# Optimization experiments

Measured on AMD Instinct MI355X. Metric: run time of the kernel, lower is better.

Reference implementation:

```python
import jax, jax.numpy as jnp
import numpy as np

SOCIAL_IDS = (1, 18)
BN_EPS = 1e-5


def conv1d(x, w, b):
    # x: [N, C, L], w: [O, I, 3], padding=1
    y = jax.lax.conv_general_dilated(x, w, window_strides=(1,), padding=[(1, 1)],
                                     dimension_numbers=("NCH", "OIH", "NCH"))
    return y + b[None, :, None]


def batchnorm(x, gamma, beta):
    # training-mode BatchNorm1d: biased stats over (N, L)
    m = x.mean(axis=(0, 2), keepdims=True)
    v = ((x - m) ** 2).mean(axis=(0, 2), keepdims=True)
    return gamma[None, :, None] * (x - m) * jax.lax.rsqrt(v + BN_EPS) + beta[None, :, None]


def social_stats(activity_ids):
    # Vectorized run-length-encoding of the social mask (replaces the per-element Python loop).
    mask = (activity_ids == SOCIAL_IDS[0]) | (activity_ids == SOCIAL_IDS[1])  # [B, S]
    prev = jnp.pad(mask[:, :-1], ((0, 0), (1, 0)))
    starts = mask & ~prev
    nseg = starts.sum(-1).astype(jnp.float32)                 # sigma_frequency
    total_dur = mask.sum(-1).astype(jnp.float32)
    mu_dur = jnp.where(nseg > 0, total_dur / jnp.maximum(nseg, 1.0), 0.0)
    # gap positions: non-social with social both before and after -> exactly the inter-segment gaps
    cum = jnp.cumsum(mask, axis=-1)
    rcum = jnp.cumsum(mask[:, ::-1], axis=-1)[:, ::-1]
    gap_sum = ((~mask) & (cum > 0) & (rcum > 0)).sum(-1).astype(jnp.float32)
    resp = jnp.where(nseg > 1, gap_sum / jnp.maximum(nseg - 1.0, 1.0), 0.0)
    return jnp.stack([mu_dur, nseg, resp], axis=-1)          # [B, 3]


def compute_sws(cur, base):
    num = cur[:, 0] * cur[:, 1]
    den = base[:, 0] * base[:, 1] + 1e-10
    return jnp.clip(1.0 - num / den, 0.0, 1.0)


def setup_inputs() -> dict:
    key = jax.random.key(0)
    ks = jax.random.split(key, 16)
    B, S, D, V = 32, 8192, 128, 21
    inp = {
        "activity_ids": jax.random.randint(ks[0], (B, S), 0, V),
        "baseline_stats": jax.random.uniform(ks[1], (B, 3), dtype=jnp.float32) * 10.0 + 0.5,
        "embed": jax.random.normal(ks[2], (V, D), dtype=jnp.float32),
        "W1": jax.random.normal(ks[3], (256, D, 3), dtype=jnp.float32) * 0.05,
        "b1": jnp.zeros((256,), jnp.float32),
        "g1": jnp.ones((256,), jnp.float32),
        "be1": jnp.zeros((256,), jnp.float32),
        "W2": jax.random.normal(ks[4], (128, 256, 3), dtype=jnp.float32) * 0.05,
        "b2": jnp.zeros((128,), jnp.float32),
        "g2": jnp.ones((128,), jnp.float32),
        "be2": jnp.zeros((128,), jnp.float32),
        "W3": jax.random.normal(ks[5], (D, 128, 3), dtype=jnp.float32) * 0.05,
        "b3": jnp.zeros((D,), jnp.float32),
        "Ws": jax.random.normal(ks[6], (D, 3), dtype=jnp.float32) * 0.1,
        "bs": jnp.zeros((D,), jnp.float32),
        "Wo": jax.random.normal(ks[7], (D, 2 * D), dtype=jnp.float32) * 0.05,
        "bo": jnp.zeros((D,), jnp.float32),
    }
    return inp


def reference(activity_ids, baseline_stats, embed, W1, b1, g1, be1, W2, b2, g2, be2,
              W3, b3, Ws, bs, Wo, bo):
    x = embed[activity_ids]                   # [B, S, D]
    x = x.transpose(0, 2, 1)                  # [B, D, S]
    x = jax.nn.relu(batchnorm(conv1d(x, W1, b1), g1, be1))
    x = jax.nn.relu(batchnorm(conv1d(x, W2, b2), g2, be2))
    x = jax.nn.relu(conv1d(x, W3, b3))
    h_cnn = x.mean(axis=2)                    # [B, D]
    stats = social_stats(activity_ids)        # [B, 3]
    h_stats = stats @ Ws.T + bs               # [B, D]
    sws = compute_sws(stats, baseline_stats)  # [B]
    h = jnp.concatenate([h_cnn, h_stats], axis=-1)
    h_si = h @ Wo.T + bo                      # [B, D]
    return (h_si, sws)
```

## Files before the change

kernel.cpp:

```cpp
#include <hip/hip_runtime.h>
#include <hip/hip_bf16.h>
#include <cstdint>
#include <cstddef>

#define B_    32
#define S_    8192
#define D_    128
#define V_    21
#define VP_   22
#define T_    (VP_*VP_*VP_)
#define TPAD_ 10656
#define C1_   256
#define C2_   128
#define NPOS_ (B_*S_)
#define CH_   128
#define NCHUNK_ 64

using bf16x8 = __attribute__((ext_vector_type(8))) short;
using f32x4  = __attribute__((ext_vector_type(4))) float;
using u32x4  = __attribute__((ext_vector_type(4))) unsigned;

__device__ inline unsigned short f2bf(float f) {
  union { float f; unsigned u; } v; v.f = f;
  unsigned r = v.u + 0x7fffu + ((v.u >> 16) & 1u);
  return (unsigned short)(r >> 16);
}
__device__ inline float bf2f(unsigned short h) {
  union { unsigned u; float f; } v; v.u = ((unsigned)h) << 16; return v.f;
}

__global__ void k_prep(const float* __restrict__ W1, const float* __restrict__ emb,
                       const float* __restrict__ W2, const float* __restrict__ W3,
                       float* __restrict__ G, unsigned short* __restrict__ Wr2,
                       unsigned short* __restrict__ W3r,
                       const int* __restrict__ ids, int* __restrict__ tIdx,
                       int* __restrict__ cnt, int* __restrict__ socC,
                       int* __restrict__ socS, int* __restrict__ socF,
                       int* __restrict__ socL) {
  int bid = blockIdx.x;
  if (bid < 66) {
    int v = bid % VP_, k = bid / VP_, o = threadIdx.x;
    __shared__ float e[D_];
    if (o < D_) e[o] = (v < V_) ? emb[v * D_ + o] : 0.f;
    __syncthreads();
    float acc = 0.f;
    if (v < V_) {
      for (int i = 0; i < D_; ++i) acc += W1[o * (D_ * 3) + i * 3 + k] * e[i];
    }
    G[(k * VP_ + v) * C1_ + o] = acc;
    return;
  }
  if (bid < 834) {
    int idx = (bid - 66) * 256 + threadIdx.x;
    if (idx < 384 * 256) {
      int r = idx >> 8, o = idx & 255;
      int k = r >> 7, p = r & 127;
      Wr2[idx] = f2bf(W2[(p * C1_ + o) * 3 + k]);
    } else {
      int j = idx - 384 * 256;
      if (j < 128 * 384) {
        int q = j / 384, kk = j % 384;
        int k = kk >> 7, p = kk & 127;
        W3r[q * 384 + kk] = f2bf(W3[(q * C2_ + p) * 3 + k]);
      }
    }
    return;
  }
  int idx = (bid - 834) * 256 + threadIdx.x;
  int b = idx >> 13, s = idx & (S_ - 1);
  const int* row = ids + b * S_;
  int a = (s > 0)      ? row[s - 1] : V_;
  int m = row[s];
  int c = (s < S_ - 1) ? row[s + 1] : V_;
  int t = (a * VP_ + m) * VP_ + c;
  tIdx[idx] = t;
  atomicAdd(&cnt[t], 1);

  bool sm = (m == 1) | (m == 18);
  bool pm = (a == 1) | (a == 18);
  unsigned long long bm = __ballot(sm);
  unsigned long long bs = __ballot(sm && !pm);
  __shared__ int l0, l1, l2, l3;
  if (threadIdx.x == 0) { l0 = 0; l1 = 0; l2 = 0; l3 = 0; }
  __syncthreads();
  int lane = threadIdx.x & 63;
  int fc = sm ? (S_ - 1 - s) : 0;
  int lv = sm ? s : 0;
#pragma unroll
  for (int off = 1; off < 64; off <<= 1) {
    fc = max(fc, __shfl_xor(fc, off));
    lv = max(lv, __shfl_xor(lv, off));
  }
  if (lane == 0) {
    atomicAdd(&l0, (int)__popcll(bm));
    atomicAdd(&l1, (int)__popcll(bs));
    atomicMax(&l2, fc);
    atomicMax(&l3, lv);
  }
  __syncthreads();
  if (threadIdx.x == 0) {
    atomicAdd(&socC[b], l0); atomicAdd(&socS[b], l1);
    atomicMax(&socF[b], l2); atomicMax(&socL[b], l3);
  }
}

__global__ void k_stats1(const float* __restrict__ G, const float* __restrict__ b1,
                         const int* __restrict__ cnt,
                         float* __restrict__ m1acc, float* __restrict__ v1acc) {
  int o = threadIdx.x;
  float bb = b1[o];
  float s = 0.f, sq = 0.f;
  int t0 = blockIdx.x * 16;
#pragma unroll 4
  for (int i = 0; i < 16; ++i) {
    int t = t0 + i;
    if (t >= T_) break;
    int a = t / (VP_ * VP_), m = (t / VP_) % VP_, c = t % VP_;
    float x = G[a * C1_ + o] + G[(VP_ + m) * C1_ + o] + G[(2 * VP_ + c) * C1_ + o] + bb;
    float w = (float)cnt[t];
    s += w * x; sq += w * x * x;
  }
  atomicAdd(&m1acc[o], s);
  atomicAdd(&v1acc[o], sq);
}

__global__ void k_z1(const float* __restrict__ G, const float* __restrict__ b1,
                     const float* __restrict__ m1a, const float* __restrict__ v1a,
                     const float* __restrict__ g1, const float* __restrict__ be1,
                     unsigned* __restrict__ Z1u) {
  int tid = threadIdx.x;
  int t = blockIdx.x * 2 + (tid >> 7);
  int o = (tid & 127) * 2;
  float m0 = m1a[o] * (1.f / NPOS_), m1v = m1a[o + 1] * (1.f / NPOS_);
  float a0 = g1[o]     * rsqrtf(v1a[o]     * (1.f / NPOS_) - m0 * m0   + 1e-5f);
  float a1 = g1[o + 1] * rsqrtf(v1a[o + 1] * (1.f / NPOS_) - m1v * m1v + 1e-5f);
  float c0 = be1[o] - m0 * a0, c1 = be1[o + 1] - m1v * a1;
  unsigned pk = 0;
  if (t < T_) {
    int a = t / (VP_ * VP_), m = (t / VP_) % VP_, c = t % VP_;
    float2 xa = *(const float2*)(G + (size_t)a * C1_ + o);
    float2 xm = *(const float2*)(G + (size_t)(VP_ + m) * C1_ + o);
    float2 xc = *(const float2*)(G + (size_t)(2 * VP_ + c) * C1_ + o);
    float x0 = xa.x + xm.x + xc.x + b1[o];
    float x1 = xa.y + xm.y + xc.y + b1[o + 1];
    float z0 = fmaxf(a0 * x0 + c0, 0.f);
    float z1 = fmaxf(a1 * x1 + c1, 0.f);
    pk = (unsigned)f2bf(z0) | ((unsigned)f2bf(z1) << 16);
  }
  Z1u[(size_t)t * 128 + (tid & 127)] = pk;
}

__global__ void __launch_bounds__(256) k_hgemm(const unsigned short* __restrict__ Z1,
                                               const unsigned short* __restrict__ Wr2,
                                               unsigned short* __restrict__ H) {
  int wave = threadIdx.x >> 6, lane = threadIdx.x & 63;
  int mt = blockIdx.x * 4 + wave;
  if (mt >= TPAD_ / 16) return;
  int nt0 = blockIdx.y * 8;
  int rc   = lane & 15;
  int kgrp = lane >> 4;
  bf16x8 af[8];
  const unsigned short* Arow = Z1 + (size_t)(mt * 16 + rc) * C1_ + kgrp * 8;
#pragma unroll
  for (int st = 0; st < 8; ++st) af[st] = *(const bf16x8*)(Arow + st * 32);
#pragma unroll
  for (int ntp = 0; ntp < 4; ++ntp) {
    int ntA = nt0 + ntp * 2, ntB = ntA + 1;
    f32x4 accA = {0.f, 0.f, 0.f, 0.f}, accB = {0.f, 0.f, 0.f, 0.f};
    const unsigned short* BrA = Wr2 + (size_t)(ntA * 16 + rc) * C1_ + kgrp * 8;
    const unsigned short* BrB = Wr2 + (size_t)(ntB * 16 + rc) * C1_ + kgrp * 8;
#pragma unroll
    for (int st = 0; st < 8; ++st) {
      bf16x8 bA = *(const bf16x8*)(BrA + st * 32);
      bf16x8 bB = *(const bf16x8*)(BrB + st * 32);
      accA = __builtin_amdgcn_mfma_f32_16x16x32_bf16(af[st], bA, accA, 0, 0, 0);
      accB = __builtin_amdgcn_mfma_f32_16x16x32_bf16(af[st], bB, accB, 0, 0, 0);
    }
#pragma unroll
    for (int r = 0; r < 4; ++r) {
      int m = mt * 16 + kgrp * 4 + r;
      H[(size_t)m * 384 + ntA * 16 + rc] = f2bf(accA[r]);
      H[(size_t)m * 384 + ntB * 16 + rc] = f2bf(accB[r]);
    }
  }
}

#define YPB 256
__global__ void __launch_bounds__(256, 3) k_y2stats(const int* __restrict__ tIdx,
        const unsigned short* __restrict__ H, const float* __restrict__ b2,
        unsigned short* __restrict__ y2, float* __restrict__ sum, float* __restrict__ sq) {
  int lane16 = threadIdx.x & 15;
  int pgrp   = threadIdx.x >> 4;
  int base0  = blockIdx.x * YPB;
  float bb[8];
  const float* b2s = b2 + lane16 * 8;
#pragma unroll
  for (int j = 0; j < 8; ++j) bb[j] = b2s[j];
  float sAcc[8] = {0,0,0,0,0,0,0,0}, qAcc[8] = {0,0,0,0,0,0,0,0};

  for (int ib = 0; ib < 2; ++ib) {
    int base = base0 + ib * 128;
    int tA[8], tM[8], tC[8];
#pragma unroll
    for (int i = 0; i < 8; ++i) {
      int pos = base + i * 16 + pgrp;
      int s = pos & (S_ - 1);
      const int* tr = tIdx + (pos & ~(S_ - 1));
      tM[i] = tr[s];
      int sa = s > 0 ? s - 1 : 0;
      int sc = s < S_ - 1 ? s + 1 : s;
      int ta = tr[sa], tc = tr[sc];
      tA[i] = (s > 0)      ? ta : T_;
      tC[i] = (s < S_ - 1) ? tc : T_;
    }
    bf16x8 h0[8], h1[8], h2[8];
#pragma unroll
    for (int i = 0; i < 8; ++i)
      h1[i] = *(const bf16x8*)(H + (size_t)tM[i] * 384 + 128 + lane16 * 8);
#pragma unroll
    for (int i = 0; i < 8; ++i)
      h0[i] = *(const bf16x8*)(H + (size_t)tA[i] * 384 +   0 + lane16 * 8);
#pragma unroll
    for (int i = 0; i < 8; ++i)
      h2[i] = *(const bf16x8*)(H + (size_t)tC[i] * 384 + 256 + lane16 * 8);

#pragma unroll
    for (int i = 0; i < 8; ++i) {
      int pos = base + i * 16 + pgrp;
      float y[8];
#pragma unroll
      for (int j = 0; j < 8; ++j) {
        y[j] = bb[j] + bf2f((unsigned short)h0[i][j]) + bf2f((unsigned short)h1[i][j])
                     + bf2f((unsigned short)h2[i][j]);
        sAcc[j] += y[j]; qAcc[j] += y[j] * y[j];
      }
      u32x4 pk;
      pk[0] = (unsigned)f2bf(y[0]) | ((unsigned)f2bf(y[1]) << 16);
      pk[1] = (unsigned)f2bf(y[2]) | ((unsigned)f2bf(y[3]) << 16);
      pk[2] = (unsigned)f2bf(y[4]) | ((unsigned)f2bf(y[5]) << 16);
      pk[3] = (unsigned)f2bf(y[6]) | ((unsigned)f2bf(y[7]) << 16);
      *(u32x4*)(y2 + (size_t)pos * C2_ + lane16 * 8) = pk;
    }
  }

  __shared__ float ls[128], lq[128];
  if (threadIdx.x < 128) { ls[threadIdx.x] = 0.f; lq[threadIdx.x] = 0.f; }
  __syncthreads();
  int lane = threadIdx.x & 63;
#pragma unroll
  for (int j = 0; j < 8; ++j) {
    float v = sAcc[j], q = qAcc[j];
    v += __shfl_xor(v, 16); v += __shfl_xor(v, 32);
    q += __shfl_xor(q, 16); q += __shfl_xor(q, 32);
    if (lane < 16) { atomicAdd(&ls[lane16 * 8 + j], v); atomicAdd(&lq[lane16 * 8 + j], q); }
  }
  __syncthreads();
  if (threadIdx.x < 128) {
    atomicAdd(&sum[threadIdx.x], ls[threadIdx.x]);
    atomicAdd(&sq[threadIdx.x],  lq[threadIdx.x]);
  }
}

__global__ void __launch_bounds__(256, 3) k_conv3(const unsigned short* __restrict__ y2,
      const float* __restrict__ s2a, const float* __restrict__ q2a,
      const float* __restrict__ g2, const float* __restrict__ be2,
      const unsigned short* __restrict__ W3r, const float* __restrict__ b3,
      float* __restrict__ part) {
  __shared__ unsigned short z2s[130 * 128];
  int b     = blockIdx.x >> 6;
  int chunk = blockIdx.x & 63;
  int s0    = chunk * CH_;
  int tid = threadIdx.x;

  {
    int lane16 = tid & 15;
    int rowg   = tid >> 4;
    const unsigned short* ybase = y2 + (size_t)b * S_ * C2_ + lane16 * 8;
    bf16x8 hv[9];
    int uu[9];
#pragma unroll
    for (int it = 0; it < 9; ++it) {
      int pos = it * 16 + rowg;
      int u = s0 - 1 + pos;
      uu[it] = u;
      int uc = min(max(u, 0), S_ - 1);
      hv[it] = *(const bf16x8*)(ybase + (size_t)uc * C2_);
    }
    float aa[8], cc[8];
#pragma unroll
    for (int j = 0; j < 8; ++j) {
      int ch = lane16 * 8 + j;
      float mm = s2a[ch] * (1.f / NPOS_);
      float vv = q2a[ch] * (1.f / NPOS_) - mm * mm;
      float a  = g2[ch] * rsqrtf(vv + 1e-5f);
      aa[j] = a; cc[j] = be2[ch] - mm * a;
    }
#pragma unroll
    for (int it = 0; it < 9; ++it) {
      int pos = it * 16 + rowg;
      bool valid = (uu[it] >= 0) & (uu[it] < S_);
      float z[8];
#pragma unroll
      for (int j = 0; j < 8; ++j)
        z[j] = fmaxf(aa[j] * bf2f((unsigned short)hv[it][j]) + cc[j], 0.f);
      u32x4 pk;
      pk[0] = (unsigned)f2bf(z[0]) | ((unsigned)f2bf(z[1]) << 16);
      pk[1] = (unsigned)f2bf(z[2]) | ((unsigned)f2bf(z[3]) << 16);
      pk[2] = (unsigned)f2bf(z[4]) | ((unsigned)f2bf(z[5]) << 16);
      pk[3] = (unsigned)f2bf(z[6]) | ((unsigned)f2bf(z[7]) << 16);
      if (!valid) pk = (u32x4){0, 0, 0, 0};
      if (pos < CH_ + 2) {
        int byte = (lane16 * 16) ^ ((pos & 15) << 4);
        *(u32x4*)((char*)z2s + pos * 256 + byte) = pk;
      }
    }
  }
  __syncthreads();

  int wave = tid >> 6, lane = tid & 63;
  int rc = lane & 15, kgrp = lane >> 4;
  int q0 = wave * 32;
  f32x4 acc[2][8];
#pragma unroll
  for (int qt = 0; qt < 2; ++qt)
#pragma unroll
    for (int nt = 0; nt < 8; ++nt) acc[qt][nt] = (f32x4){0.f, 0.f, 0.f, 0.f};

  const unsigned short* A0 = W3r + (size_t)(q0 +  0 + rc) * 384 + kgrp * 8;
  const unsigned short* A1 = W3r + (size_t)(q0 + 16 + rc) * 384 + kgrp * 8;
#pragma unroll
  for (int kh = 0; kh < 2; ++kh) {
    bf16x8 af0[6], af1[6];
#pragma unroll
    for (int s6 = 0; s6 < 6; ++s6) {
      af0[s6] = *(const bf16x8*)(A0 + (kh * 6 + s6) * 32);
      af1[s6] = *(const bf16x8*)(A1 + (kh * 6 + s6) * 32);
    }
#pragma unroll
    for (int s6 = 0; s6 < 6; ++s6) {
      int st = kh * 6 + s6;
      int k = st >> 2, pb = st & 3;
      int pbyte = pb * 64 + kgrp * 16;
#pragma unroll
      for (int nt = 0; nt < 8; ++nt) {
        int pos  = nt * 16 + rc + k;
        bf16x8 bfr = *(const bf16x8*)((const char*)z2s + pos * 256 + (pbyte ^ ((pos & 15) << 4)));
        acc[0][nt] = __builtin_amdgcn_mfma_f32_16x16x32_bf16(af0[s6], bfr, acc[0][nt], 0, 0, 0);
        acc[1][nt] = __builtin_amdgcn_mfma_f32_16x16x32_bf16(af1[s6], bfr, acc[1][nt], 0, 0, 0);
      }
    }
  }

#pragma unroll
  for (int qt = 0; qt < 2; ++qt) {
    float p[4];
    const float4 b3q = *(const float4*)(b3 + q0 + qt * 16 + kgrp * 4);
#pragma unroll
    for (int r = 0; r < 4; ++r) p[r] = 0.f;
#pragma unroll
    for (int nt = 0; nt < 8; ++nt) {
      p[0] += fmaxf(acc[qt][nt][0] + b3q.x, 0.f);
      p[1] += fmaxf(acc[qt][nt][1] + b3q.y, 0.f);
      p[2] += fmaxf(acc[qt][nt][2] + b3q.z, 0.f);
      p[3] += fmaxf(acc[qt][nt][3] + b3q.w, 0.f);
    }
#pragma unroll
    for (int off = 1; off < 16; off <<= 1) {
      p[0] += __shfl_xor(p[0], off); p[1] += __shfl_xor(p[1], off);
      p[2] += __shfl_xor(p[2], off); p[3] += __shfl_xor(p[3], off);
    }
    if (rc == 0) {
      float* dst = part + ((size_t)b * NCHUNK_ + chunk) * C2_ + q0 + qt * 16 + kgrp * 4;
      dst[0] = p[0]; dst[1] = p[1]; dst[2] = p[2]; dst[3] = p[3];
    }
  }
}

__global__ void k_final(const float* __restrict__ part,
      const int* __restrict__ socC, const int* __restrict__ socS,
      const int* __restrict__ socF, const int* __restrict__ socL,
      const float* __restrict__ baseline,
      const float* __restrict__ Ws, const float* __restrict__ bs,
      const float* __restrict__ Wo, const float* __restrict__ bo,
      float* __restrict__ out) {
  int b = blockIdx.x, q = threadIdx.x;
  __shared__ float h[256];
  __shared__ float st3[3];
  {
    float acc = 0.f;
    const float* pb = part + (size_t)b * NCHUNK_ * C2_ + q;
#pragma unroll 8
    for (int i = 0; i < NCHUNK_; ++i) acc += pb[i * C2_];
    h[q] = acc * (1.f / S_);
  }
  if (q == 0) {
    float total = (float)socC[b], nseg = (float)socS[b];
    int first = (S_ - 1) - socF[b], last = socL[b];
    float mu   = (nseg > 0.f) ? total / fmaxf(nseg, 1.f) : 0.f;
    float gap  = (nseg > 0.f) ? (float)(last - first + 1) - total : 0.f;
    float resp = (nseg > 1.f) ? gap / fmaxf(nseg - 1.f, 1.f) : 0.f;
    st3[0] = mu; st3[1] = nseg; st3[2] = resp;
    float den = baseline[b * 3 + 0] * baseline[b * 3 + 1] + 1e-10f;
    float sws = 1.f - mu * nseg / den;
    out[B_ * C2_ + b] = fminf(fmaxf(sws, 0.f), 1.f);
  }
  __syncthreads();
  h[128 + q] = Ws[q * 3] * st3[0] + Ws[q * 3 + 1] * st3[1] + Ws[q * 3 + 2] * st3[2] + bs[q];
  __syncthreads();
  float acc = bo[q];
  const float4* Wo4 = (const float4*)(Wo + q * 256);
#pragma unroll 8
  for (int j4 = 0; j4 < 64; ++j4) {
    float4 wv = Wo4[j4];
    acc += wv.x * h[j4 * 4] + wv.y * h[j4 * 4 + 1] + wv.z * h[j4 * 4 + 2] + wv.w * h[j4 * 4 + 3];
  }
  out[b * C2_ + q] = acc;
}

extern "C" void kernel_launch(void* const* d_in, const int* in_sizes, int n_in,
                              void* d_out, int out_size, void* d_ws, size_t ws_size,
                              hipStream_t stream) {
  const int*   ids = (const int*)  d_in[0];
  const float* bas = (const float*)d_in[1];
  const float* emb = (const float*)d_in[2];
  const float* W1  = (const float*)d_in[3];
  const float* b1  = (const float*)d_in[4];
  const float* g1  = (const float*)d_in[5];
  const float* be1 = (const float*)d_in[6];
  const float* W2  = (const float*)d_in[7];
  const float* b2  = (const float*)d_in[8];
  const float* g2  = (const float*)d_in[9];
  const float* be2 = (const float*)d_in[10];
  const float* W3  = (const float*)d_in[11];
  const float* b3  = (const float*)d_in[12];
  const float* Ws  = (const float*)d_in[13];
  const float* bs  = (const float*)d_in[14];
  const float* Wo  = (const float*)d_in[15];
  const float* bo  = (const float*)d_in[16];
  float* out = (float*)d_out;

  char* w = (char*)d_ws;
  size_t off = 0;
  auto alloc = [&](size_t bytes) -> size_t {
    size_t o = off; off = (off + bytes + 255) & ~(size_t)255; return o;
  };
  size_t o_cnt  = alloc(T_ * 4);
  size_t o_m1   = alloc(C1_ * 4);
  size_t o_v1   = alloc(C1_ * 4);
  size_t o_s2   = alloc(C2_ * 4);
  size_t o_q2   = alloc(C2_ * 4);
  size_t o_socC = alloc(B_ * 4);
  size_t o_socS = alloc(B_ * 4);
  size_t o_socF = alloc(B_ * 4);
  size_t o_socL = alloc(B_ * 4);
  size_t zeroEnd = off;
  size_t o_part = alloc((size_t)B_ * NCHUNK_ * C2_ * 4);
  size_t o_tidx = alloc((size_t)NPOS_ * 4);
  size_t o_G    = alloc((size_t)3 * VP_ * C1_ * 4);
  size_t o_Z1   = alloc((size_t)TPAD_ * C1_ * 2);
  size_t o_Wr2  = alloc((size_t)384 * 256 * 2);
  size_t o_W3r  = alloc((size_t)128 * 384 * 2);
  size_t o_H    = alloc((size_t)TPAD_ * 384 * 2);
  size_t o_y2   = alloc((size_t)NPOS_ * C2_ * 2);
  (void)ws_size; (void)n_in; (void)in_sizes; (void)out_size;

  int*            cnt  = (int*)(w + o_cnt);
  float*          m1a  = (float*)(w + o_m1);
  float*          v1a  = (float*)(w + o_v1);
  float*          s2a  = (float*)(w + o_s2);
  float*          q2a  = (float*)(w + o_q2);
  int*            socC = (int*)(w + o_socC);
  int*            socS = (int*)(w + o_socS);
  int*            socF = (int*)(w + o_socF);
  int*            socL = (int*)(w + o_socL);
  float*          part = (float*)(w + o_part);
  int*            tIdx = (int*)(w + o_tidx);
  float*          G    = (float*)(w + o_G);
  unsigned short* Z1   = (unsigned short*)(w + o_Z1);
  unsigned short* Wr2  = (unsigned short*)(w + o_Wr2);
  unsigned short* W3r  = (unsigned short*)(w + o_W3r);
  unsigned short* H    = (unsigned short*)(w + o_H);
  unsigned short* y2   = (unsigned short*)(w + o_y2);

  hipMemsetAsync(w, 0, zeroEnd, stream);

  k_prep    <<<834 + NPOS_ / 256, 256, 0, stream>>>(W1, emb, W2, W3, G, Wr2, W3r,
                                                    ids, tIdx, cnt, socC, socS, socF, socL);
  k_stats1  <<<(T_ + 15) / 16, 256, 0, stream>>>(G, b1, cnt, m1a, v1a);
  k_z1      <<<TPAD_ / 2, 256, 0, stream>>>(G, b1, m1a, v1a, g1, be1, (unsigned*)Z1);
  k_hgemm   <<<dim3((TPAD_ / 16 + 3) / 4, 3), 256, 0, stream>>>(Z1, Wr2, H);
  k_y2stats <<<NPOS_ / YPB, 256, 0, stream>>>(tIdx, H, b2, y2, s2a, q2a);
  k_conv3   <<<B_ * NCHUNK_, 256, 0, stream>>>(y2, s2a, q2a, g2, be2, W3r, b3, part);
  k_final   <<<B_, 128, 0, stream>>>(part, socC, socS, socF, socL, bas, Ws, bs, Wo, bo, out);
}
```

Measured before the change: 266.6 us.

## Fuse BN1 into GEMM prologue and recompute conv2 outputs instead of storing y2

```diff
diff --git a/kernel.cpp b/kernel.cpp
--- a/kernel.cpp
+++ b/kernel.cpp
@@ -15,6 +15,7 @@
 #define NPOS_ (B_*S_)
 #define CH_   128
 #define NCHUNK_ 64
+#define NSET_ 32
 
 using bf16x8 = __attribute__((ext_vector_type(8))) short;
 using f32x4  = __attribute__((ext_vector_type(4))) float;
@@ -104,65 +105,76 @@
   }
 }
 
-__global__ void k_stats1(const float* __restrict__ G, const float* __restrict__ b1,
-                         const int* __restrict__ cnt,
-                         float* __restrict__ m1acc, float* __restrict__ v1acc) {
+__global__ void k_stats1(const float* __restrict__ G, const int* __restrict__ cnt,
+                         const float* __restrict__ g1, const float* __restrict__ be1,
+                         float* __restrict__ m1acc, float* __restrict__ v1acc,
+                         int* __restrict__ done, float* __restrict__ a1,
+                         float* __restrict__ c1) {
   int o = threadIdx.x;
-  float bb = b1[o];
   float s = 0.f, sq = 0.f;
-  int t0 = blockIdx.x * 16;
+  int t0 = blockIdx.x * 64;
 #pragma unroll 4
-  for (int i = 0; i < 16; ++i) {
+  for (int i = 0; i < 64; ++i) {
     int t = t0 + i;
-    if (t >= T_) break;
-    int a = t / (VP_ * VP_), m = (t / VP_) % VP_, c = t % VP_;
-    float x = G[a * C1_ + o] + G[(VP_ + m) * C1_ + o] + G[(2 * VP_ + c) * C1_ + o] + bb;
-    float w = (float)cnt[t];
-    s += w * x; sq += w * x * x;
+    if (t < T_) {
+      int a = t / (VP_ * VP_), m = (t / VP_) % VP_, c = t % VP_;
+      float x = G[a * C1_ + o] + G[(VP_ + m) * C1_ + o] + G[(2 * VP_ + c) * C1_ + o];
+      float wgt = (float)cnt[t];
+      s += wgt * x; sq += wgt * x * x;
+    }
   }
   atomicAdd(&m1acc[o], s);
   atomicAdd(&v1acc[o], sq);
-}
-
-__global__ void k_z1(const float* __restrict__ G, const float* __restrict__ b1,
-                     const float* __restrict__ m1a, const float* __restrict__ v1a,
-                     const float* __restrict__ g1, const float* __restrict__ be1,
-                     unsigned* __restrict__ Z1u) {
-  int tid = threadIdx.x;
-  int t = blockIdx.x * 2 + (tid >> 7);
-  int o = (tid & 127) * 2;
-  float m0 = m1a[o] * (1.f / NPOS_), m1v = m1a[o + 1] * (1.f / NPOS_);
-  float a0 = g1[o]     * rsqrtf(v1a[o]     * (1.f / NPOS_) - m0 * m0   + 1e-5f);
-  float a1 = g1[o + 1] * rsqrtf(v1a[o + 1] * (1.f / NPOS_) - m1v * m1v + 1e-5f);
-  float c0 = be1[o] - m0 * a0, c1 = be1[o + 1] - m1v * a1;
-  unsigned pk = 0;
-  if (t < T_) {
-    int a = t / (VP_ * VP_), m = (t / VP_) % VP_, c = t % VP_;
-    float2 xa = *(const float2*)(G + (size_t)a * C1_ + o);
-    float2 xm = *(const float2*)(G + (size_t)(VP_ + m) * C1_ + o);
-    float2 xc = *(const float2*)(G + (size_t)(2 * VP_ + c) * C1_ + o);
-    float x0 = xa.x + xm.x + xc.x + b1[o];
-    float x1 = xa.y + xm.y + xc.y + b1[o + 1];
-    float z0 = fmaxf(a0 * x0 + c0, 0.f);
-    float z1 = fmaxf(a1 * x1 + c1, 0.f);
-    pk = (unsigned)f2bf(z0) | ((unsigned)f2bf(z1) << 16);
-  }
-  Z1u[(size_t)t * 128 + (tid & 127)] = pk;
-}
-
-__global__ void __launch_bounds__(256) k_hgemm(const unsigned short* __restrict__ Z1,
-                                               const unsigned short* __restrict__ Wr2,
-                                               unsigned short* __restrict__ H) {
+  __syncthreads();
+  __shared__ int lastFlag;
+  if (o == 0) lastFlag = (atomicAdd(done, 1) == (int)gridDim.x - 1);
+  __syncthreads();
+  if (lastFlag) {
+    float ms = atomicAdd(&m1acc[o], 0.f);
+    float vs = atomicAdd(&v1acc[o], 0.f);
+    float mu  = ms * (1.f / NPOS_);
+    float var = vs * (1.f / NPOS_) - mu * mu;
+    float a   = g1[o] * rsqrtf(var + 1e-5f);
+    a1[o] = a; c1[o] = be1[o] - mu * a;
+  }
+}
+
+__global__ void __launch_bounds__(256) k_hgemm(const float* __restrict__ G,
+      const float* __restrict__ a1, const float* __restrict__ c1,
+      const unsigned short* __restrict__ Wr2, unsigned short* __restrict__ H) {
   int wave = threadIdx.x >> 6, lane = threadIdx.x & 63;
   int mt = blockIdx.x * 4 + wave;
   if (mt >= TPAD_ / 16) return;
   int nt0 = blockIdx.y * 8;
   int rc   = lane & 15;
   int kgrp = lane >> 4;
+  int t = mt * 16 + rc;
   bf16x8 af[8];
-  const unsigned short* Arow = Z1 + (size_t)(mt * 16 + rc) * C1_ + kgrp * 8;
-#pragma unroll
-  for (int st = 0; st < 8; ++st) af[st] = *(const bf16x8*)(Arow + st * 32);
+  if (t < T_) {
+    int a = t / (VP_ * VP_), m = (t / VP_) % VP_, c = t % VP_;
+    const float* Ga = G + (size_t)a * C1_;
+    const float* Gm = G + (size_t)(VP_ + m) * C1_;
+    const float* Gc = G + (size_t)(2 * VP_ + c) * C1_;
+#pragma unroll
+    for (int st = 0; st < 8; ++st) {
+      int o0 = kgrp * 8 + st * 32;
+#pragma unroll
+      for (int j4 = 0; j4 < 2; ++j4) {
+        float4 xa = *(const float4*)(Ga + o0 + j4 * 4);
+        float4 xm = *(const float4*)(Gm + o0 + j4 * 4);
+        float4 xc = *(const float4*)(Gc + o0 + j4 * 4);
+        float4 av = *(const float4*)(a1 + o0 + j4 * 4);
+        float4 cv = *(const float4*)(c1 + o0 + j4 * 4);
+        af[st][j4 * 4 + 0] = (short)f2bf(fmaxf(av.x * (xa.x + xm.x + xc.x) + cv.x, 0.f));
+        af[st][j4 * 4 + 1] = (short)f2bf(fmaxf(av.y * (xa.y + xm.y + xc.y) + cv.y, 0.f));
+        af[st][j4 * 4 + 2] = (short)f2bf(fmaxf(av.z * (xa.z + xm.z + xc.z) + cv.z, 0.f));
+        af[st][j4 * 4 + 3] = (short)f2bf(fmaxf(av.w * (xa.w + xm.w + xc.w) + cv.w, 0.f));
+      }
+    }
+  } else {
+#pragma unroll
+    for (int st = 0; st < 8; ++st) af[st] = (bf16x8){0, 0, 0, 0, 0, 0, 0, 0};
+  }
 #pragma unroll
   for (int ntp = 0; ntp < 4; ++ntp) {
     int ntA = nt0 + ntp * 2, ntB = ntA + 1;
@@ -178,75 +190,60 @@
     }
 #pragma unroll
     for (int r = 0; r < 4; ++r) {
-      int m = mt * 16 + kgrp * 4 + r;
-      H[(size_t)m * 384 + ntA * 16 + rc] = f2bf(accA[r]);
-      H[(size_t)m * 384 + ntB * 16 + rc] = f2bf(accB[r]);
-    }
-  }
-}
-
-#define YPB 256
-__global__ void __launch_bounds__(256, 3) k_y2stats(const int* __restrict__ tIdx,
-        const unsigned short* __restrict__ H, const float* __restrict__ b2,
-        unsigned short* __restrict__ y2, float* __restrict__ sum, float* __restrict__ sq) {
-  int lane16 = threadIdx.x & 15;
-  int pgrp   = threadIdx.x >> 4;
-  int base0  = blockIdx.x * YPB;
-  float bb[8];
-  const float* b2s = b2 + lane16 * 8;
-#pragma unroll
-  for (int j = 0; j < 8; ++j) bb[j] = b2s[j];
+      int mrow = mt * 16 + kgrp * 4 + r;
+      H[(size_t)mrow * 384 + ntA * 16 + rc] = f2bf(accA[r]);
+      H[(size_t)mrow * 384 + ntB * 16 + rc] = f2bf(accB[r]);
+    }
+  }
+}
+
+__global__ void k_stats2(const int* __restrict__ tIdx, const unsigned short* __restrict__ H,
+        float* __restrict__ s2p, float* __restrict__ q2p, int* __restrict__ done,
+        const float* __restrict__ g2, const float* __restrict__ be2,
+        float* __restrict__ a2, float* __restrict__ c2p) {
+  int tid = threadIdx.x;
+  int lane16 = tid & 15;
+  int pgrp   = tid >> 4;
+  int base   = blockIdx.x * 128;
+  int tA[8], tM[8], tC[8];
+#pragma unroll
+  for (int i = 0; i < 8; ++i) {
+    int pos = base + i * 16 + pgrp;
+    int s = pos & (S_ - 1);
+    const int* tr = tIdx + (pos & ~(S_ - 1));
+    tM[i] = tr[s];
+    int sa = s > 0 ? s - 1 : 0;
+    int sc = s < S_ - 1 ? s + 1 : s;
+    int ta = tr[sa], tc = tr[sc];
+    tA[i] = (s > 0)      ? ta : T_;
+    tC[i] = (s < S_ - 1) ? tc : T_;
+  }
+  bf16x8 h0[8], h1[8], h2[8];
+#pragma unroll
+  for (int i = 0; i < 8; ++i)
+    h1[i] = *(const bf16x8*)(H + (size_t)tM[i] * 384 + 128 + lane16 * 8);
+#pragma unroll
+  for (int i = 0; i < 8; ++i)
+    h0[i] = *(const bf16x8*)(H + (size_t)tA[i] * 384 +   0 + lane16 * 8);
+#pragma unroll
+  for (int i = 0; i < 8; ++i)
+    h2[i] = *(const bf16x8*)(H + (size_t)tC[i] * 384 + 256 + lane16 * 8);
+
   float sAcc[8] = {0,0,0,0,0,0,0,0}, qAcc[8] = {0,0,0,0,0,0,0,0};
-
-  for (int ib = 0; ib < 2; ++ib) {
-    int base = base0 + ib * 128;
-    int tA[8], tM[8], tC[8];
-#pragma unroll
-    for (int i = 0; i < 8; ++i) {
-      int pos = base + i * 16 + pgrp;
-      int s = pos & (S_ - 1);
-      const int* tr = tIdx + (pos & ~(S_ - 1));
-      tM[i] = tr[s];
-      int sa = s > 0 ? s - 1 : 0;
-      int sc = s < S_ - 1 ? s + 1 : s;
-      int ta = tr[sa], tc = tr[sc];
-      tA[i] = (s > 0)      ? ta : T_;
-      tC[i] = (s < S_ - 1) ? tc : T_;
-    }
-    bf16x8 h0[8], h1[8], h2[8];
-#pragma unroll
-    for (int i = 0; i < 8; ++i)
-      h1[i] = *(const bf16x8*)(H + (size_t)tM[i] * 384 + 128 + lane16 * 8);
-#pragma unroll
-    for (int i = 0; i < 8; ++i)
-      h0[i] = *(const bf16x8*)(H + (size_t)tA[i] * 384 +   0 + lane16 * 8);
-#pragma unroll
-    for (int i = 0; i < 8; ++i)
-      h2[i] = *(const bf16x8*)(H + (size_t)tC[i] * 384 + 256 + lane16 * 8);
-
-#pragma unroll
-    for (int i = 0; i < 8; ++i) {
-      int pos = base + i * 16 + pgrp;
-      float y[8];
-#pragma unroll
-      for (int j = 0; j < 8; ++j) {
-        y[j] = bb[j] + bf2f((unsigned short)h0[i][j]) + bf2f((unsigned short)h1[i][j])
-                     + bf2f((unsigned short)h2[i][j]);
-        sAcc[j] += y[j]; qAcc[j] += y[j] * y[j];
-      }
-      u32x4 pk;
-      pk[0] = (unsigned)f2bf(y[0]) | ((unsigned)f2bf(y[1]) << 16);
-      pk[1] = (unsigned)f2bf(y[2]) | ((unsigned)f2bf(y[3]) << 16);
-      pk[2] = (unsigned)f2bf(y[4]) | ((unsigned)f2bf(y[5]) << 16);
-      pk[3] = (unsigned)f2bf(y[6]) | ((unsigned)f2bf(y[7]) << 16);
-      *(u32x4*)(y2 + (size_t)pos * C2_ + lane16 * 8) = pk;
+#pragma unroll
+  for (int i = 0; i < 8; ++i) {
+#pragma unroll
+    for (int j = 0; j < 8; ++j) {
+      float y = bf2f((unsigned short)h0[i][j]) + bf2f((unsigned short)h1[i][j])
+              + bf2f((unsigned short)h2[i][j]);
+      sAcc[j] += y; qAcc[j] += y * y;
     }
   }
 
   __shared__ float ls[128], lq[128];
-  if (threadIdx.x < 128) { ls[threadIdx.x] = 0.f; lq[threadIdx.x] = 0.f; }
-  __syncthreads();
-  int lane = threadIdx.x & 63;
+  if (tid < 128) { ls[tid] = 0.f; lq[tid] = 0.f; }
+  __syncthreads();
+  int lane = tid & 63;
 #pragma unroll
   for (int j = 0; j < 8; ++j) {
     float v = sAcc[j], q = qAcc[j];
@@ -255,15 +252,31 @@
     if (lane < 16) { atomicAdd(&ls[lane16 * 8 + j], v); atomicAdd(&lq[lane16 * 8 + j], q); }
   }
   __syncthreads();
-  if (threadIdx.x < 128) {
-    atomicAdd(&sum[threadIdx.x], ls[threadIdx.x]);
-    atomicAdd(&sq[threadIdx.x],  lq[threadIdx.x]);
-  }
-}
-
-__global__ void __launch_bounds__(256, 3) k_conv3(const unsigned short* __restrict__ y2,
-      const float* __restrict__ s2a, const float* __restrict__ q2a,
-      const float* __restrict__ g2, const float* __restrict__ be2,
+  int set = (blockIdx.x & (NSET_ - 1)) * C2_;
+  if (tid < 128) {
+    atomicAdd(&s2p[set + tid], ls[tid]);
+    atomicAdd(&q2p[set + tid], lq[tid]);
+  }
+  __syncthreads();
+  __shared__ int lastFlag;
+  if (tid == 0) lastFlag = (atomicAdd(done, 1) == (int)gridDim.x - 1);
+  __syncthreads();
+  if (lastFlag && tid < 128) {
+    float s = 0.f, q = 0.f;
+    for (int k2 = 0; k2 < NSET_; ++k2) {
+      s += atomicAdd(&s2p[k2 * C2_ + tid], 0.f);
+      q += atomicAdd(&q2p[k2 * C2_ + tid], 0.f);
+    }
+    float mu  = s * (1.f / NPOS_);
+    float var = q * (1.f / NPOS_) - mu * mu;
+    float a   = g2[tid] * rsqrtf(var + 1e-5f);
+    a2[tid] = a; c2p[tid] = be2[tid] - mu * a;
+  }
+}
+
+__global__ void __launch_bounds__(256, 3) k_conv3(const int* __restrict__ tIdx,
+      const unsigned short* __restrict__ H,
+      const float* __restrict__ a2, const float* __restrict__ c2p,
       const unsigned short* __restrict__ W3r, const float* __restrict__ b3,
       float* __restrict__ part) {
   __shared__ unsigned short z2s[130 * 128];
@@ -274,44 +287,72 @@
 
   {
     int lane16 = tid & 15;
-    int rowg   = tid >> 4;
-    const unsigned short* ybase = y2 + (size_t)b * S_ * C2_ + lane16 * 8;
-    bf16x8 hv[9];
-    int uu[9];
-#pragma unroll
-    for (int it = 0; it < 9; ++it) {
-      int pos = it * 16 + rowg;
-      int u = s0 - 1 + pos;
-      uu[it] = u;
-      int uc = min(max(u, 0), S_ - 1);
-      hv[it] = *(const bf16x8*)(ybase + (size_t)uc * C2_);
-    }
+    int pgrp   = tid >> 4;
+    const int* tr = tIdx + b * S_;
     float aa[8], cc[8];
 #pragma unroll
-    for (int j = 0; j < 8; ++j) {
-      int ch = lane16 * 8 + j;
-      float mm = s2a[ch] * (1.f / NPOS_);
-      float vv = q2a[ch] * (1.f / NPOS_) - mm * mm;
-      float a  = g2[ch] * rsqrtf(vv + 1e-5f);
-      aa[j] = a; cc[j] = be2[ch] - mm * a;
-    }
-#pragma unroll
-    for (int it = 0; it < 9; ++it) {
-      int pos = it * 16 + rowg;
-      bool valid = (uu[it] >= 0) & (uu[it] < S_);
-      float z[8];
-#pragma unroll
-      for (int j = 0; j < 8; ++j)
-        z[j] = fmaxf(aa[j] * bf2f((unsigned short)hv[it][j]) + cc[j], 0.f);
-      u32x4 pk;
-      pk[0] = (unsigned)f2bf(z[0]) | ((unsigned)f2bf(z[1]) << 16);
-      pk[1] = (unsigned)f2bf(z[2]) | ((unsigned)f2bf(z[3]) << 16);
-      pk[2] = (unsigned)f2bf(z[4]) | ((unsigned)f2bf(z[5]) << 16);
-      pk[3] = (unsigned)f2bf(z[6]) | ((unsigned)f2bf(z[7]) << 16);
-      if (!valid) pk = (u32x4){0, 0, 0, 0};
-      if (pos < CH_ + 2) {
-        int byte = (lane16 * 16) ^ ((pos & 15) << 4);
-        *(u32x4*)((char*)z2s + pos * 256 + byte) = pk;
+    for (int j4 = 0; j4 < 2; ++j4) {
+      float4 av = *(const float4*)(a2  + lane16 * 8 + j4 * 4);
+      float4 cv = *(const float4*)(c2p + lane16 * 8 + j4 * 4);
+      aa[j4 * 4 + 0] = av.x; aa[j4 * 4 + 1] = av.y;
+      aa[j4 * 4 + 2] = av.z; aa[j4 * 4 + 3] = av.w;
+      cc[j4 * 4 + 0] = cv.x; cc[j4 * 4 + 1] = cv.y;
+      cc[j4 * 4 + 2] = cv.z; cc[j4 * 4 + 3] = cv.w;
+    }
+#pragma unroll
+    for (int half = 0; half < 2; ++half) {
+      const int i0 = half * 5;
+      const int NB = half ? 4 : 5;
+      int uu[5], iA[5], iM[5], iC[5];
+#pragma unroll
+      for (int i = 0; i < 5; ++i) {
+        if (i >= NB) break;
+        int pos = (i0 + i) * 16 + pgrp;
+        int u = s0 - 1 + pos;
+        int uc = min(max(u, 0), S_ - 1);
+        uu[i] = u;
+        iM[i] = tr[uc];
+        iA[i] = (uc > 0)      ? tr[uc - 1] : T_;
+        iC[i] = (uc < S_ - 1) ? tr[uc + 1] : T_;
+      }
+      bf16x8 h0[5], h1[5], h2[5];
+#pragma unroll
+      for (int i = 0; i < 5; ++i) {
+        if (i >= NB) break;
+        h1[i] = *(const bf16x8*)(H + (size_t)iM[i] * 384 + 128 + lane16 * 8);
+      }
+#pragma unroll
+      for (int i = 0; i < 5; ++i) {
+        if (i >= NB) break;
+        h0[i] = *(const bf16x8*)(H + (size_t)iA[i] * 384 +   0 + lane16 * 8);
+      }
+#pragma unroll
+      for (int i = 0; i < 5; ++i) {
+        if (i >= NB) break;
+        h2[i] = *(const bf16x8*)(H + (size_t)iC[i] * 384 + 256 + lane16 * 8);
+      }
+#pragma unroll
+      for (int i = 0; i < 5; ++i) {
+        if (i >= NB) break;
+        int pos = (i0 + i) * 16 + pgrp;
+        bool valid = (uu[i] >= 0) & (uu[i] < S_);
+        float z[8];
+#pragma unroll
+        for (int j = 0; j < 8; ++j) {
+          float y = bf2f((unsigned short)h0[i][j]) + bf2f((unsigned short)h1[i][j])
+                  + bf2f((unsigned short)h2[i][j]);
+          z[j] = fmaxf(aa[j] * y + cc[j], 0.f);
+        }
+        u32x4 pk;
+        pk[0] = (unsigned)f2bf(z[0]) | ((unsigned)f2bf(z[1]) << 16);
+        pk[1] = (unsigned)f2bf(z[2]) | ((unsigned)f2bf(z[3]) << 16);
+        pk[2] = (unsigned)f2bf(z[4]) | ((unsigned)f2bf(z[5]) << 16);
+        pk[3] = (unsigned)f2bf(z[6]) | ((unsigned)f2bf(z[7]) << 16);
+        if (!valid) pk = (u32x4){0, 0, 0, 0};
+        if (pos < CH_ + 2) {
+          int byte = (lane16 * 16) ^ ((pos & 15) << 4);
+          *(u32x4*)((char*)z2s + pos * 256 + byte) = pk;
+        }
       }
     }
   }
@@ -424,11 +465,9 @@
   const float* bas = (const float*)d_in[1];
   const float* emb = (const float*)d_in[2];
   const float* W1  = (const float*)d_in[3];
-  const float* b1  = (const float*)d_in[4];
   const float* g1  = (const float*)d_in[5];
   const float* be1 = (const float*)d_in[6];
   const float* W2  = (const float*)d_in[7];
-  const float* b2  = (const float*)d_in[8];
   const float* g2  = (const float*)d_in[9];
   const float* be2 = (const float*)d_in[10];
   const float* W3  = (const float*)d_in[11];
@@ -444,52 +483,59 @@
   auto alloc = [&](size_t bytes) -> size_t {
     size_t o = off; off = (off + bytes + 255) & ~(size_t)255; return o;
   };
-  size_t o_cnt  = alloc(T_ * 4);
-  size_t o_m1   = alloc(C1_ * 4);
-  size_t o_v1   = alloc(C1_ * 4);
-  size_t o_s2   = alloc(C2_ * 4);
-  size_t o_q2   = alloc(C2_ * 4);
-  size_t o_socC = alloc(B_ * 4);
-  size_t o_socS = alloc(B_ * 4);
-  size_t o_socF = alloc(B_ * 4);
-  size_t o_socL = alloc(B_ * 4);
+  size_t o_cnt   = alloc(T_ * 4);
+  size_t o_m1    = alloc(C1_ * 4);
+  size_t o_v1    = alloc(C1_ * 4);
+  size_t o_s2p   = alloc((size_t)NSET_ * C2_ * 4);
+  size_t o_q2p   = alloc((size_t)NSET_ * C2_ * 4);
+  size_t o_socC  = alloc(B_ * 4);
+  size_t o_socS  = alloc(B_ * 4);
+  size_t o_socF  = alloc(B_ * 4);
+  size_t o_socL  = alloc(B_ * 4);
+  size_t o_done1 = alloc(256);
+  size_t o_done2 = alloc(256);
   size_t zeroEnd = off;
-  size_t o_part = alloc((size_t)B_ * NCHUNK_ * C2_ * 4);
-  size_t o_tidx = alloc((size_t)NPOS_ * 4);
-  size_t o_G    = alloc((size_t)3 * VP_ * C1_ * 4);
-  size_t o_Z1   = alloc((size_t)TPAD_ * C1_ * 2);
-  size_t o_Wr2  = alloc((size_t)384 * 256 * 2);
-  size_t o_W3r  = alloc((size_t)128 * 384 * 2);
-  size_t o_H    = alloc((size_t)TPAD_ * 384 * 2);
-  size_t o_y2   = alloc((size_t)NPOS_ * C2_ * 2);
+  size_t o_part  = alloc((size_t)B_ * NCHUNK_ * C2_ * 4);
+  size_t o_tidx  = alloc((size_t)NPOS_ * 4);
+  size_t o_G     = alloc((size_t)3 * VP_ * C1_ * 4);
+  size_t o_Wr2   = alloc((size_t)384 * 256 * 2);
+  size_t o_W3r   = alloc((size_t)128 * 384 * 2);
+  size_t o_H     = alloc((size_t)TPAD_ * 384 * 2);
+  size_t o_a1    = alloc(C1_ * 4);
+  size_t o_c1    = alloc(C1_ * 4);
+  size_t o_a2    = alloc(C2_ * 4);
+  size_t o_c2    = alloc(C2_ * 4);
   (void)ws_size; (void)n_in; (void)in_sizes; (void)out_size;
 
   int*            cnt  = (int*)(w + o_cnt);
   float*          m1a  = (float*)(w + o_m1);
   float*          v1a  = (float*)(w + o_v1);
-  float*          s2a  = (float*)(w + o_s2);
-  float*          q2a  = (float*)(w + o_q2);
+  float*          s2p  = (float*)(w + o_s2p);
+  float*          q2p  = (float*)(w + o_q2p);
   int*            socC = (int*)(w + o_socC);
   int*            socS = (int*)(w + o_socS);
   int*            socF = (int*)(w + o_socF);
   int*            socL = (int*)(w + o_socL);
+  int*            dn1  = (int*)(w + o_done1);
+  int*            dn2  = (int*)(w + o_done2);
   float*          part = (float*)(w + o_part);
   int*            tIdx = (int*)(w + o_tidx);
   float*          G    = (float*)(w + o_G);
-  unsigned short* Z1   = (unsigned short*)(w + o_Z1);
   unsigned short* Wr2  = (unsigned short*)(w + o_Wr2);
   unsigned short* W3r  = (unsigned short*)(w + o_W3r);
   unsigned short* H    = (unsigned short*)(w + o_H);
-  unsigned short* y2   = (unsigned short*)(w + o_y2);
+  float*          a1   = (float*)(w + o_a1);
+  float*          c1   = (float*)(w + o_c1);
+  float*          a2   = (float*)(w + o_a2);
+  float*          c2p  = (float*)(w + o_c2);
 
   hipMemsetAsync(w, 0, zeroEnd, stream);
 
-  k_prep    <<<834 + NPOS_ / 256, 256, 0, stream>>>(W1, emb, W2, W3, G, Wr2, W3r,
-                                                    ids, tIdx, cnt, socC, socS, socF, socL);
-  k_stats1  <<<(T_ + 15) / 16, 256, 0, stream>>>(G, b1, cnt, m1a, v1a);
-  k_z1      <<<TPAD_ / 2, 256, 0, stream>>>(G, b1, m1a, v1a, g1, be1, (unsigned*)Z1);
-  k_hgemm   <<<dim3((TPAD_ / 16 + 3) / 4, 3), 256, 0, stream>>>(Z1, Wr2, H);
-  k_y2stats <<<NPOS_ / YPB, 256, 0, stream>>>(tIdx, H, b2, y2, s2a, q2a);
-  k_conv3   <<<B_ * NCHUNK_, 256, 0, stream>>>(y2, s2a, q2a, g2, be2, W3r, b3, part);
-  k_final   <<<B_, 128, 0, stream>>>(part, socC, socS, socF, socL, bas, Ws, bs, Wo, bo, out);
-}
+  k_prep  <<<834 + NPOS_ / 256, 256, 0, stream>>>(W1, emb, W2, W3, G, Wr2, W3r,
+                                                  ids, tIdx, cnt, socC, socS, socF, socL);
+  k_stats1<<<(T_ + 63) / 64, 256, 0, stream>>>(G, cnt, g1, be1, m1a, v1a, dn1, a1, c1);
+  k_hgemm <<<dim3((TPAD_ / 16 + 3) / 4, 3), 256, 0, stream>>>(G, a1, c1, Wr2, H);
+  k_stats2<<<NPOS_ / 128, 256, 0, stream>>>(tIdx, H, s2p, q2p, dn2, g2, be2, a2, c2p);
+  k_conv3 <<<B_ * NCHUNK_, 256, 0, stream>>>(tIdx, H, a2, c2p, W3r, b3, part);
+  k_final <<<B_, 128, 0, stream>>>(part, socC, socS, socF, socL, bas, Ws, bs, Wo, bo, out);
+}
```

Measured after the change: 249.8 us. -6.3%, faster.
